# Kernel tuning notes

Hardware: AMD Instinct MI355X
Metric: run time of the kernel (lower is better)

The kernel has to match this reference:

```python
import jax, jax.numpy as jnp
import numpy as np

B, T, IN, H, NCLS = 128, 500, 306, 512, 4


def setup_inputs() -> dict:
    key = jax.random.key(0)
    ks = jax.random.split(key, 12)
    s_in = 1.0 / np.sqrt(H)  # PyTorch RNN init scale: U(-1/sqrt(H), 1/sqrt(H))
    u = lambda k, shape: jax.random.uniform(k, shape, jnp.float32, -s_in, s_in)
    return {
        "x": jax.random.normal(ks[0], (B, T, IN), jnp.float32),
        "W_ih0": u(ks[1], (H, IN)),
        "W_hh0": u(ks[2], (H, H)),
        "b_ih0": u(ks[3], (H,)),
        "b_hh0": u(ks[4], (H,)),
        "W_ih1": u(ks[5], (H, H)),
        "W_hh1": u(ks[6], (H, H)),
        "b_ih1": u(ks[7], (H,)),
        "b_hh1": u(ks[8], (H,)),
        "W_fc": u(ks[9], (NCLS, H)),
        "b_fc": u(ks[10], (NCLS,)),
    }


def _rnn_layer(inp, W_ih, W_hh, b_ih, b_hh):
    # Precompute input contribution for all timesteps: [B, T, H]
    pre = jnp.einsum('bti,hi->bth', inp, W_ih) + b_ih + b_hh
    h0 = jnp.zeros((inp.shape[0], W_hh.shape[0]), inp.dtype)

    def step(h, p_t):  # p_t: [B, H]
        h_new = jnp.tanh(p_t + h @ W_hh.T)
        return h_new, h_new

    _, hs = jax.lax.scan(step, h0, jnp.swapaxes(pre, 0, 1))  # hs: [T, B, H]
    return jnp.swapaxes(hs, 0, 1)  # [B, T, H]


def reference(x, W_ih0, W_hh0, b_ih0, b_hh0, W_ih1, W_hh1, b_ih1, b_hh1, W_fc, b_fc):
    h = _rnn_layer(x, W_ih0, W_hh0, b_ih0, b_hh0)
    h = _rnn_layer(h, W_ih1, W_hh1, b_ih1, b_hh1)
    last = h[:, -1, :]                      # [B, H]
    logits = last @ W_fc.T + b_fc           # [B, NCLS]
    return jax.nn.softmax(logits, axis=1)
```

## Files before the change

### kernel.cpp

```cpp
#include <hip/hip_runtime.h>
#include <cstdint>
#include <cstddef>

#define Bb   128
#define Tt   500
#define INn  306
#define Hh   512
#define GRID 128
#define BH32 (Bb * Hh)

typedef short bf16x8 __attribute__((ext_vector_type(8)));
typedef float f32x4  __attribute__((ext_vector_type(4)));
typedef unsigned u32x4 __attribute__((ext_vector_type(4)));
typedef unsigned short u16t;

union F8 { bf16x8 v; uint4 q; unsigned u[4]; u16t s[8]; };

__device__ __forceinline__ float bf2f(u16t h) {
  unsigned u = ((unsigned)h) << 16;
  return __builtin_bit_cast(float, u);
}
__device__ __forceinline__ u16t f2bf(float f) {
  unsigned u = __builtin_bit_cast(unsigned, f);
  unsigned r = u + 0x7fffu + ((u >> 16) & 1u);
  return (u16t)(r >> 16);
}
__device__ __forceinline__ void splitRNE(float v, u16t& hi, u16t& lo) {
  hi = f2bf(v);
  lo = f2bf(v - bf2f(hi));
}
__device__ __forceinline__ void splitTR(float v, u16t& hi, u16t& lo) {
  unsigned u = __builtin_bit_cast(unsigned, v);
  hi = (u16t)(u >> 16);
  float hf = __builtin_bit_cast(float, u & 0xFFFF0000u);
  lo = (u16t)(__builtin_bit_cast(unsigned, v - hf) >> 16);
}
__device__ __forceinline__ f32x4 MF(const F8& a, const F8& b, f32x4 c) {
  return __builtin_amdgcn_mfma_f32_16x16x32_bf16(a.v, b.v, c, 0, 0, 0);
}

__device__ __forceinline__ void stw(unsigned* p, unsigned v) {
  __hip_atomic_store(p, v, __ATOMIC_RELAXED, __HIP_MEMORY_SCOPE_AGENT);
}
__device__ __forceinline__ unsigned ldw(const unsigned* p) {
  return __hip_atomic_load(p, __ATOMIC_RELAXED, __HIP_MEMORY_SCOPE_AGENT);
}


template<bool FAST>
__device__ __forceinline__ void stf(unsigned* p, unsigned v) {
  if constexpr (FAST) *(volatile unsigned*)p = v;
  else stw(p, v);
}
template<bool FAST>
__device__ __forceinline__ void invL() {
  if constexpr (FAST) asm volatile("buffer_inv" ::: "memory");
  else asm volatile("buffer_inv sc1" ::: "memory");
}
template<bool FAST>
__device__ __forceinline__ void fpoll(const unsigned* p, unsigned v) {
  if constexpr (FAST) {
    for (;;) {
      asm volatile("buffer_inv" ::: "memory");
      if (*(const volatile unsigned*)p == v) break;
      __builtin_amdgcn_s_sleep(1);
    }
  } else {
    while (ldw(p) != v) __builtin_amdgcn_s_sleep(1);
  }
}

__device__ __forceinline__ void stage_tile(const unsigned* __restrict__ gsrc,
                                           unsigned char* smHi,
                                           unsigned char* smLo, int tid) {
  const int row = tid >> 4;
  const int c0  = tid & 15;
#pragma unroll
  for (int k = 0; k < 8; ++k) {
    const int cg = c0 + k * 16;
    const u32x4 w = *(const u32x4*)(gsrc + (size_t)row * Hh + (size_t)cg * 4);
    const unsigned hi0 = (w[1] & 0xFFFF0000u) | (w[0] >> 16);
    const unsigned hi1 = (w[3] & 0xFFFF0000u) | (w[2] >> 16);
    const unsigned lo0 = (w[1] << 16) | (w[0] & 0xFFFFu);
    const unsigned lo1 = (w[3] << 16) | (w[2] & 0xFFFFu);
    const int ch   = cg >> 1;
    const int half = cg & 1;
    const size_t boff = (size_t)row * 1024 + ((size_t)(ch ^ (row & 7)) << 4)
                      + (size_t)half * 8;
    *(uint2*)(smHi + boff) = make_uint2(hi0, hi1);
    *(uint2*)(smLo + boff) = make_uint2(lo0, lo1);
  }
}
__device__ __forceinline__ F8 fragLDS(const unsigned char* smP, int row,
                                      int kc, int quad) {
  const int c = kc * 4 + quad;
  F8 f;
  f.q = *(const uint4*)(smP + (size_t)row * 1024
                        + ((size_t)(c ^ (row & 7)) << 4));
  return f;
}

template<bool FAST>
__device__ void body(
    const float* x,
    const float* Wih0, const float* Whh0, const float* bih0, const float* bhh0,
    const float* Wih1, const float* Whh1, const float* bih1, const float* bhh1,
    const float* Wfc,  const float* bfc, float* out,
    unsigned* fl, unsigned* h0p, unsigned* h1p, unsigned char* sm,
    int sub, int tid, int Mb)
{
  const int lane = tid & 63;
  const int wave = tid >> 6;
  const int l15  = lane & 15;
  const int quad = lane >> 4;

  unsigned char* smA = sm;
  unsigned char* smB = sm + 16384;
  unsigned char* smC = sm + 32768;
  unsigned char* smD = sm + 49152;

  const bool isL0 = (sub < 8);
  const int Jb    = (isL0 ? sub : sub - 8) * 64;
  const int jn    = Jb + wave * 16 + l15;
  const int rowA  = Mb + l15;
  const int mOutB = Mb + quad * 4;

  if (isL0) {
    F8 Bxh[10], Bxl[10], Bhh[16], Bhl[16];
#pragma unroll
    for (int kc = 0; kc < 10; ++kc) {
#pragma unroll
      for (int e = 0; e < 8; ++e) {
        const int k = kc * 32 + quad * 8 + e;
        float v = (k < INn) ? Wih0[(size_t)jn * INn + k] : 0.f;
        splitRNE(v, Bxh[kc].s[e], Bxl[kc].s[e]);
      }
    }
#pragma unroll
    for (int kc = 0; kc < 16; ++kc) {
      const float* wr = Whh0 + (size_t)jn * Hh + kc * 32 + quad * 8;
#pragma unroll
      for (int e = 0; e < 8; ++e)
        splitRNE(wr[e], Bhh[kc].s[e], Bhl[kc].s[e]);
    }
    const float bv = bih0[jn] + bhh0[jn];

    for (int t = 0; t < Tt; ++t) {
      F8 xh[10], xl[10];
      {
        const float* xr = x + ((size_t)rowA * Tt + t) * INn;
#pragma unroll
        for (int kc = 0; kc < 10; ++kc) {
          const int kb = kc * 32 + quad * 8;
          float v[8];
          if (kc < 9) {
            const float2* p = (const float2*)(xr + kb);
#pragma unroll
            for (int h2 = 0; h2 < 4; ++h2) {
              float2 w = p[h2];
              v[2 * h2] = w.x; v[2 * h2 + 1] = w.y;
            }
          } else {
#pragma unroll
            for (int e = 0; e < 8; ++e)
              v[e] = (kb + e < INn) ? xr[kb + e] : 0.f;
          }
#pragma unroll
          for (int e = 0; e < 8; ++e) splitTR(v[e], xh[kc].s[e], xl[kc].s[e]);
        }
      }

      if (t >= 1) {
        asm volatile("s_waitcnt vmcnt(0)" ::: "memory");
        __syncthreads();
        if (tid == 0) stf<FAST>(fl + sub * 2 + ((t - 1) & 1), (unsigned)t);
      }
      if (t >= 1 && tid < 8)
        fpoll<FAST>(fl + tid * 2 + ((t - 1) & 1), (unsigned)t);
      if (t >= 2 && tid >= 8 && tid < 16)
        fpoll<FAST>(fl + tid * 2 + ((t - 2) & 1), (unsigned)(t - 1));
      __syncthreads();
      invL<FAST>();

      if (t >= 1) {
        stage_tile(h0p + (size_t)((t - 1) & 1) * BH32 + (size_t)Mb * Hh,
                   smA, smB, tid);
        __syncthreads();
      }
      f32x4 ac0 = {bv, bv, bv, bv};
      f32x4 ac1 = {0.f, 0.f, 0.f, 0.f};
      f32x4 ac2 = {0.f, 0.f, 0.f, 0.f};
      if (t >= 1) {
#pragma unroll
        for (int kc = 0; kc < 16; ++kc) {
          F8 ah = fragLDS(smA, l15, kc, quad);
          F8 al = fragLDS(smB, l15, kc, quad);
          ac0 = MF(ah, Bhh[kc], ac0);
          ac1 = MF(ah, Bhl[kc], ac1);
          ac2 = MF(al, Bhh[kc], ac2);
        }
      }
#pragma unroll
      for (int kc = 0; kc < 10; ++kc) {
        ac0 = MF(xh[kc], Bxh[kc], ac0);
        ac1 = MF(xh[kc], Bxl[kc], ac1);
        ac2 = MF(xl[kc], Bxh[kc], ac2);
      }

      unsigned* dst = h0p + (size_t)(t & 1) * BH32;
#pragma unroll
      for (int r = 0; r < 4; ++r) {
        const float v = tanhf(ac0[r] + ac1[r] + ac2[r]);
        u16t hb, lb; splitRNE(v, hb, lb);
        stf<FAST>(dst + (size_t)(mOutB + r) * Hh + jn,
                  ((unsigned)hb << 16) | (unsigned)lb);
      }
    }
    asm volatile("s_waitcnt vmcnt(0)" ::: "memory");
    __syncthreads();
    if (tid == 0) stf<FAST>(fl + sub * 2 + ((Tt - 1) & 1), (unsigned)Tt);
  } else {
    F8 Bih[16], Bil[16], Bh2[16], Bl2[16];
#pragma unroll
    for (int kc = 0; kc < 16; ++kc) {
      const float* w1 = Wih1 + (size_t)jn * Hh + kc * 32 + quad * 8;
      const float* w2 = Whh1 + (size_t)jn * Hh + kc * 32 + quad * 8;
#pragma unroll
      for (int e = 0; e < 8; ++e) {
        splitRNE(w1[e], Bih[kc].s[e], Bil[kc].s[e]);
        splitRNE(w2[e], Bh2[kc].s[e], Bl2[kc].s[e]);
      }
    }
    const float bv = bih1[jn] + bhh1[jn];

    for (int t = 0; t < Tt; ++t) {
      if (tid < 8)
        fpoll<FAST>(fl + tid * 2 + (t & 1), (unsigned)(t + 1));
      if (t >= 1) {
        asm volatile("s_waitcnt vmcnt(0)" ::: "memory");
        __syncthreads();
        if (tid == 0) stf<FAST>(fl + sub * 2 + ((t - 1) & 1), (unsigned)t);
        if (tid >= 8 && tid < 16)
          fpoll<FAST>(fl + tid * 2 + ((t - 1) & 1), (unsigned)t);
      }
      __syncthreads();
      invL<FAST>();

      stage_tile(h0p + (size_t)(t & 1) * BH32 + (size_t)Mb * Hh,
                 smA, smB, tid);
      if (t >= 1)
        stage_tile(h1p + (size_t)((t - 1) & 1) * BH32 + (size_t)Mb * Hh,
                   smC, smD, tid);
      __syncthreads();

      f32x4 ac0 = {bv, bv, bv, bv};
      f32x4 ac1 = {0.f, 0.f, 0.f, 0.f};
      f32x4 ac2 = {0.f, 0.f, 0.f, 0.f};
#pragma unroll
      for (int kc = 0; kc < 16; ++kc) {
        F8 ah = fragLDS(smA, l15, kc, quad);
        F8 al = fragLDS(smB, l15, kc, quad);
        ac0 = MF(ah, Bih[kc], ac0);
        ac1 = MF(ah, Bil[kc], ac1);
        ac2 = MF(al, Bih[kc], ac2);
      }
      if (t >= 1) {
#pragma unroll
        for (int kc = 0; kc < 16; ++kc) {
          F8 ah = fragLDS(smC, l15, kc, quad);
          F8 al = fragLDS(smD, l15, kc, quad);
          ac0 = MF(ah, Bh2[kc], ac0);
          ac1 = MF(ah, Bl2[kc], ac1);
          ac2 = MF(al, Bh2[kc], ac2);
        }
      }

      unsigned* dst = h1p + (size_t)(t & 1) * BH32;
#pragma unroll
      for (int r = 0; r < 4; ++r) {
        const float v = tanhf(ac0[r] + ac1[r] + ac2[r]);
        u16t hb, lb; splitRNE(v, hb, lb);
        stf<FAST>(dst + (size_t)(mOutB + r) * Hh + jn,
                  ((unsigned)hb << 16) | (unsigned)lb);
      }
    }
    asm volatile("s_waitcnt vmcnt(0)" ::: "memory");
    __syncthreads();
    if (tid == 0) stf<FAST>(fl + sub * 2 + ((Tt - 1) & 1), (unsigned)Tt);

    if (sub == 8) {
      if (tid < 8)
        fpoll<FAST>(fl + (8 + tid) * 2 + ((Tt - 1) & 1), (unsigned)Tt);
      __syncthreads();
      invL<FAST>();
      if (tid < 16) {
        const int b = Mb + tid;
        const unsigned* hp = h1p + (size_t)((Tt - 1) & 1) * BH32
                           + (size_t)b * Hh;
        float acc[4] = {bfc[0], bfc[1], bfc[2], bfc[3]};
        for (int j = 0; j < Hh; ++j) {
          const unsigned w = *(const volatile unsigned*)(hp + j);
          const float hv = bf2f((u16t)(w >> 16)) + bf2f((u16t)(w & 0xFFFFu));
#pragma unroll
          for (int cc = 0; cc < 4; ++cc) acc[cc] += hv * Wfc[cc * Hh + j];
        }
        const float mx = fmaxf(fmaxf(acc[0], acc[1]), fmaxf(acc[2], acc[3]));
        const float e0 = expf(acc[0] - mx), e1 = expf(acc[1] - mx);
        const float e2 = expf(acc[2] - mx), e3 = expf(acc[3] - mx);
        const float si = 1.f / (e0 + e1 + e2 + e3);
        out[b * 4 + 0] = e0 * si;
        out[b * 4 + 1] = e1 * si;
        out[b * 4 + 2] = e2 * si;
        out[b * 4 + 3] = e3 * si;
      }
    }
  }
}

__global__ __launch_bounds__(256, 1) void rnn_all(
    const float* x,
    const float* Wih0, const float* Whh0, const float* bih0, const float* bhh0,
    const float* Wih1, const float* Whh1, const float* bih1, const float* bhh1,
    const float* Wfc,  const float* bfc,
    float* out, unsigned char* ws)
{
  const int wg  = blockIdx.x;
  const int g   = wg & 7;
  const int sub = wg >> 3;
  const int tid = threadIdx.x;

  __shared__ __align__(16) unsigned char sm[65536];

  unsigned* fl  = (unsigned*)(ws + (size_t)g * 128);
  unsigned* h0p = (unsigned*)(ws + 1024);
  unsigned* h1p = h0p + (size_t)2 * BH32;
  const int Mb  = g * 16;

  unsigned xcc;
  asm("s_getreg_b32 %0, hwreg(HW_REG_XCC_ID)" : "=s"(xcc));
  xcc &= 7u;
  unsigned* xt = h1p + (size_t)1 * BH32 + (size_t)Mb * Hh;
  if (tid == 0) stw(xt + sub, 0xA5C30000u | xcc);
  unsigned* xsh = (unsigned*)sm;
  if (tid < 16) {
    unsigned v;
    do { v = ldw(xt + tid); } while ((v & 0xFFFFFFF8u) != 0xA5C30000u);
    xsh[tid] = v & 7u;
  }
  __syncthreads();
  bool fast = true;
  for (int i = 0; i < 16; ++i) fast = fast && (xsh[i] == xcc);
  __syncthreads();

  if (fast)
    body<true >(x, Wih0, Whh0, bih0, bhh0, Wih1, Whh1, bih1, bhh1,
                Wfc, bfc, out, fl, h0p, h1p, sm, sub, tid, Mb);
  else
    body<false>(x, Wih0, Whh0, bih0, bhh0, Wih1, Whh1, bih1, bhh1,
                Wfc, bfc, out, fl, h0p, h1p, sm, sub, tid, Mb);
}

extern "C" void kernel_launch(void* const* d_in, const int* in_sizes, int n_in,
                              void* d_out, int out_size, void* d_ws, size_t ws_size,
                              hipStream_t stream) {
  const float* x    = (const float*)d_in[0];
  const float* Wih0 = (const float*)d_in[1];
  const float* Whh0 = (const float*)d_in[2];
  const float* bih0 = (const float*)d_in[3];
  const float* bhh0 = (const float*)d_in[4];
  const float* Wih1 = (const float*)d_in[5];
  const float* Whh1 = (const float*)d_in[6];
  const float* bih1 = (const float*)d_in[7];
  const float* bhh1 = (const float*)d_in[8];
  const float* Wfc  = (const float*)d_in[9];
  const float* bfc  = (const float*)d_in[10];
  float* out = (float*)d_out;
  unsigned char* ws = (unsigned char*)d_ws;

  rnn_all<<<dim3(GRID), dim3(256), 0, stream>>>(
      x, Wih0, Whh0, bih0, bhh0, Wih1, Whh1, bih1, bhh1, Wfc, bfc, out, ws);
}
```

Before: 5.150 ms.

## Co-locate layer-0 and layer-1 waves in each workgroup with skewed wavefront schedule

Each workgroup now holds both layers: waves 0-1 compute a 32-column slice of layer 0 and waves 2-3 a 32-column slice of layer 1, with layer 1 lagging one timestep behind. All 16 workgroups in a batch group follow one uniform barrier and flag protocol over T+1 steps, and the staged h0 tile is shared by both layers through LDS. The aim is to balance work across workgroups, drop the separate two-phase polling, and reuse one staged h0 copy for both layers. In exchange each wave keeps 64 weight fragments in registers, and every workgroup now waits on all 15 peers per step.

```diff
diff --git a/kernel.cpp b/kernel.cpp
--- a/kernel.cpp
+++ b/kernel.cpp
@@ -113,27 +113,26 @@
   const int wave = tid >> 6;
   const int l15  = lane & 15;
   const int quad = lane >> 4;
+  const bool isL0 = (wave < 2);
 
   unsigned char* smA = sm;
   unsigned char* smB = sm + 16384;
   unsigned char* smC = sm + 32768;
   unsigned char* smD = sm + 49152;
 
-  const bool isL0 = (sub < 8);
-  const int Jb    = (isL0 ? sub : sub - 8) * 64;
-  const int jn    = Jb + wave * 16 + l15;
-  const int rowA  = Mb + l15;
+  const int jn    = sub * 32 + (wave & 1) * 16 + l15;
   const int mOutB = Mb + quad * 4;
 
+  F8 W[64];
+  float bv;
   if (isL0) {
-    F8 Bxh[10], Bxl[10], Bhh[16], Bhl[16];
 #pragma unroll
     for (int kc = 0; kc < 10; ++kc) {
 #pragma unroll
       for (int e = 0; e < 8; ++e) {
         const int k = kc * 32 + quad * 8 + e;
         float v = (k < INn) ? Wih0[(size_t)jn * INn + k] : 0.f;
-        splitRNE(v, Bxh[kc].s[e], Bxl[kc].s[e]);
+        splitRNE(v, W[kc].s[e], W[10 + kc].s[e]);
       }
     }
 #pragma unroll
@@ -141,178 +140,161 @@
       const float* wr = Whh0 + (size_t)jn * Hh + kc * 32 + quad * 8;
 #pragma unroll
       for (int e = 0; e < 8; ++e)
-        splitRNE(wr[e], Bhh[kc].s[e], Bhl[kc].s[e]);
-    }
-    const float bv = bih0[jn] + bhh0[jn];
-
-    for (int t = 0; t < Tt; ++t) {
-      F8 xh[10], xl[10];
-      {
-        const float* xr = x + ((size_t)rowA * Tt + t) * INn;
+        splitRNE(wr[e], W[20 + kc].s[e], W[36 + kc].s[e]);
+    }
+    bv = bih0[jn] + bhh0[jn];
+  } else {
+#pragma unroll
+    for (int kc = 0; kc < 16; ++kc) {
+      const float* w1 = Wih1 + (size_t)jn * Hh + kc * 32 + quad * 8;
+      const float* w2 = Whh1 + (size_t)jn * Hh + kc * 32 + quad * 8;
+#pragma unroll
+      for (int e = 0; e < 8; ++e) {
+        splitRNE(w1[e], W[kc].s[e], W[16 + kc].s[e]);
+        splitRNE(w2[e], W[32 + kc].s[e], W[48 + kc].s[e]);
+      }
+    }
+    bv = bih1[jn] + bhh1[jn];
+  }
+
+  const int rowA = Mb + l15;
+
+  for (int t = 0; t <= Tt; ++t) {
+    F8 xh[10], xl[10];
+    if (isL0 && t < Tt) {
+      const float* xr = x + ((size_t)rowA * Tt + t) * INn;
+#pragma unroll
+      for (int kc = 0; kc < 10; ++kc) {
+        const int kb = kc * 32 + quad * 8;
+        float v[8];
+        if (kc < 9) {
+          const float2* p = (const float2*)(xr + kb);
+#pragma unroll
+          for (int h2 = 0; h2 < 4; ++h2) {
+            float2 w = p[h2];
+            v[2 * h2] = w.x; v[2 * h2 + 1] = w.y;
+          }
+        } else {
+#pragma unroll
+          for (int e = 0; e < 8; ++e)
+            v[e] = (kb + e < INn) ? xr[kb + e] : 0.f;
+        }
+#pragma unroll
+        for (int e = 0; e < 8; ++e) splitTR(v[e], xh[kc].s[e], xl[kc].s[e]);
+      }
+    }
+
+    asm volatile("s_waitcnt vmcnt(0)" ::: "memory");
+    __syncthreads();
+    if (t >= 1 && tid == 0)
+      stf<FAST>(fl + sub * 2 + ((t - 1) & 1), (unsigned)t);
+
+    if (t >= 1 && tid < 16 && tid != sub)
+      fpoll<FAST>(fl + tid * 2 + ((t - 1) & 1), (unsigned)t);
+    __syncthreads();
+    invL<FAST>();
+
+    if (t >= 1)
+      stage_tile(h0p + (size_t)((t - 1) & 1) * BH32 + (size_t)Mb * Hh,
+                 smA, smB, tid);
+    if (t >= 2)
+      stage_tile(h1p + (size_t)((t - 2) & 1) * BH32 + (size_t)Mb * Hh,
+                 smC, smD, tid);
+    __syncthreads();
+
+    if (isL0) {
+      if (t < Tt) {
+        f32x4 ac0 = {bv, bv, bv, bv};
+        f32x4 ac1 = {0.f, 0.f, 0.f, 0.f};
+        f32x4 ac2 = {0.f, 0.f, 0.f, 0.f};
+        if (t >= 1) {
+#pragma unroll
+          for (int kc = 0; kc < 16; ++kc) {
+            F8 ah = fragLDS(smA, l15, kc, quad);
+            F8 al = fragLDS(smB, l15, kc, quad);
+            ac0 = MF(ah, W[20 + kc], ac0);
+            ac1 = MF(ah, W[36 + kc], ac1);
+            ac2 = MF(al, W[20 + kc], ac2);
+          }
+        }
 #pragma unroll
         for (int kc = 0; kc < 10; ++kc) {
-          const int kb = kc * 32 + quad * 8;
-          float v[8];
-          if (kc < 9) {
-            const float2* p = (const float2*)(xr + kb);
-#pragma unroll
-            for (int h2 = 0; h2 < 4; ++h2) {
-              float2 w = p[h2];
-              v[2 * h2] = w.x; v[2 * h2 + 1] = w.y;
-            }
-          } else {
-#pragma unroll
-            for (int e = 0; e < 8; ++e)
-              v[e] = (kb + e < INn) ? xr[kb + e] : 0.f;
-          }
-#pragma unroll
-          for (int e = 0; e < 8; ++e) splitTR(v[e], xh[kc].s[e], xl[kc].s[e]);
-        }
-      }
-
+          ac0 = MF(xh[kc], W[kc], ac0);
+          ac1 = MF(xh[kc], W[10 + kc], ac1);
+          ac2 = MF(xl[kc], W[kc], ac2);
+        }
+        unsigned* dst = h0p + (size_t)(t & 1) * BH32;
+#pragma unroll
+        for (int r = 0; r < 4; ++r) {
+          const float v = tanhf(ac0[r] + ac1[r] + ac2[r]);
+          u16t hb, lb; splitRNE(v, hb, lb);
+          stf<FAST>(dst + (size_t)(mOutB + r) * Hh + jn,
+                    ((unsigned)hb << 16) | (unsigned)lb);
+        }
+      }
+    } else {
       if (t >= 1) {
-        asm volatile("s_waitcnt vmcnt(0)" ::: "memory");
-        __syncthreads();
-        if (tid == 0) stf<FAST>(fl + sub * 2 + ((t - 1) & 1), (unsigned)t);
-      }
-      if (t >= 1 && tid < 8)
-        fpoll<FAST>(fl + tid * 2 + ((t - 1) & 1), (unsigned)t);
-      if (t >= 2 && tid >= 8 && tid < 16)
-        fpoll<FAST>(fl + tid * 2 + ((t - 2) & 1), (unsigned)(t - 1));
-      __syncthreads();
-      invL<FAST>();
-
-      if (t >= 1) {
-        stage_tile(h0p + (size_t)((t - 1) & 1) * BH32 + (size_t)Mb * Hh,
-                   smA, smB, tid);
-        __syncthreads();
-      }
-      f32x4 ac0 = {bv, bv, bv, bv};
-      f32x4 ac1 = {0.f, 0.f, 0.f, 0.f};
-      f32x4 ac2 = {0.f, 0.f, 0.f, 0.f};
-      if (t >= 1) {
+        f32x4 ac0 = {bv, bv, bv, bv};
+        f32x4 ac1 = {0.f, 0.f, 0.f, 0.f};
+        f32x4 ac2 = {0.f, 0.f, 0.f, 0.f};
 #pragma unroll
         for (int kc = 0; kc < 16; ++kc) {
           F8 ah = fragLDS(smA, l15, kc, quad);
           F8 al = fragLDS(smB, l15, kc, quad);
-          ac0 = MF(ah, Bhh[kc], ac0);
-          ac1 = MF(ah, Bhl[kc], ac1);
-          ac2 = MF(al, Bhh[kc], ac2);
-        }
-      }
-#pragma unroll
-      for (int kc = 0; kc < 10; ++kc) {
-        ac0 = MF(xh[kc], Bxh[kc], ac0);
-        ac1 = MF(xh[kc], Bxl[kc], ac1);
-        ac2 = MF(xl[kc], Bxh[kc], ac2);
-      }
-
-      unsigned* dst = h0p + (size_t)(t & 1) * BH32;
-#pragma unroll
-      for (int r = 0; r < 4; ++r) {
-        const float v = tanhf(ac0[r] + ac1[r] + ac2[r]);
-        u16t hb, lb; splitRNE(v, hb, lb);
-        stf<FAST>(dst + (size_t)(mOutB + r) * Hh + jn,
-                  ((unsigned)hb << 16) | (unsigned)lb);
-      }
-    }
-    asm volatile("s_waitcnt vmcnt(0)" ::: "memory");
+          ac0 = MF(ah, W[kc], ac0);
+          ac1 = MF(ah, W[16 + kc], ac1);
+          ac2 = MF(al, W[kc], ac2);
+        }
+        if (t >= 2) {
+#pragma unroll
+          for (int kc = 0; kc < 16; ++kc) {
+            F8 ah = fragLDS(smC, l15, kc, quad);
+            F8 al = fragLDS(smD, l15, kc, quad);
+            ac0 = MF(ah, W[32 + kc], ac0);
+            ac1 = MF(ah, W[48 + kc], ac1);
+            ac2 = MF(al, W[32 + kc], ac2);
+          }
+        }
+        unsigned* dst = h1p + (size_t)((t - 1) & 1) * BH32;
+#pragma unroll
+        for (int r = 0; r < 4; ++r) {
+          const float v = tanhf(ac0[r] + ac1[r] + ac2[r]);
+          u16t hb, lb; splitRNE(v, hb, lb);
+          stf<FAST>(dst + (size_t)(mOutB + r) * Hh + jn,
+                    ((unsigned)hb << 16) | (unsigned)lb);
+        }
+      }
+    }
+  }
+
+  asm volatile("s_waitcnt vmcnt(0)" ::: "memory");
+  __syncthreads();
+  if (tid == 0) stf<FAST>(fl + sub * 2 + (Tt & 1), (unsigned)(Tt + 1));
+
+  if (sub == 0) {
+    if (tid < 16 && tid != 0)
+      fpoll<FAST>(fl + tid * 2 + (Tt & 1), (unsigned)(Tt + 1));
     __syncthreads();
-    if (tid == 0) stf<FAST>(fl + sub * 2 + ((Tt - 1) & 1), (unsigned)Tt);
-  } else {
-    F8 Bih[16], Bil[16], Bh2[16], Bl2[16];
-#pragma unroll
-    for (int kc = 0; kc < 16; ++kc) {
-      const float* w1 = Wih1 + (size_t)jn * Hh + kc * 32 + quad * 8;
-      const float* w2 = Whh1 + (size_t)jn * Hh + kc * 32 + quad * 8;
-#pragma unroll
-      for (int e = 0; e < 8; ++e) {
-        splitRNE(w1[e], Bih[kc].s[e], Bil[kc].s[e]);
-        splitRNE(w2[e], Bh2[kc].s[e], Bl2[kc].s[e]);
-      }
-    }
-    const float bv = bih1[jn] + bhh1[jn];
-
-    for (int t = 0; t < Tt; ++t) {
-      if (tid < 8)
-        fpoll<FAST>(fl + tid * 2 + (t & 1), (unsigned)(t + 1));
-      if (t >= 1) {
-        asm volatile("s_waitcnt vmcnt(0)" ::: "memory");
-        __syncthreads();
-        if (tid == 0) stf<FAST>(fl + sub * 2 + ((t - 1) & 1), (unsigned)t);
-        if (tid >= 8 && tid < 16)
-          fpoll<FAST>(fl + tid * 2 + ((t - 1) & 1), (unsigned)t);
-      }
-      __syncthreads();
-      invL<FAST>();
-
-      stage_tile(h0p + (size_t)(t & 1) * BH32 + (size_t)Mb * Hh,
-                 smA, smB, tid);
-      if (t >= 1)
-        stage_tile(h1p + (size_t)((t - 1) & 1) * BH32 + (size_t)Mb * Hh,
-                   smC, smD, tid);
-      __syncthreads();
-
-      f32x4 ac0 = {bv, bv, bv, bv};
-      f32x4 ac1 = {0.f, 0.f, 0.f, 0.f};
-      f32x4 ac2 = {0.f, 0.f, 0.f, 0.f};
-#pragma unroll
-      for (int kc = 0; kc < 16; ++kc) {
-        F8 ah = fragLDS(smA, l15, kc, quad);
-        F8 al = fragLDS(smB, l15, kc, quad);
-        ac0 = MF(ah, Bih[kc], ac0);
-        ac1 = MF(ah, Bil[kc], ac1);
-        ac2 = MF(al, Bih[kc], ac2);
-      }
-      if (t >= 1) {
-#pragma unroll
-        for (int kc = 0; kc < 16; ++kc) {
-          F8 ah = fragLDS(smC, l15, kc, quad);
-          F8 al = fragLDS(smD, l15, kc, quad);
-          ac0 = MF(ah, Bh2[kc], ac0);
-          ac1 = MF(ah, Bl2[kc], ac1);
-          ac2 = MF(al, Bh2[kc], ac2);
-        }
-      }
-
-      unsigned* dst = h1p + (size_t)(t & 1) * BH32;
-#pragma unroll
-      for (int r = 0; r < 4; ++r) {
-        const float v = tanhf(ac0[r] + ac1[r] + ac2[r]);
-        u16t hb, lb; splitRNE(v, hb, lb);
-        stf<FAST>(dst + (size_t)(mOutB + r) * Hh + jn,
-                  ((unsigned)hb << 16) | (unsigned)lb);
-      }
-    }
-    asm volatile("s_waitcnt vmcnt(0)" ::: "memory");
-    __syncthreads();
-    if (tid == 0) stf<FAST>(fl + sub * 2 + ((Tt - 1) & 1), (unsigned)Tt);
-
-    if (sub == 8) {
-      if (tid < 8)
-        fpoll<FAST>(fl + (8 + tid) * 2 + ((Tt - 1) & 1), (unsigned)Tt);
-      __syncthreads();
-      invL<FAST>();
-      if (tid < 16) {
-        const int b = Mb + tid;
-        const unsigned* hp = h1p + (size_t)((Tt - 1) & 1) * BH32
-                           + (size_t)b * Hh;
-        float acc[4] = {bfc[0], bfc[1], bfc[2], bfc[3]};
-        for (int j = 0; j < Hh; ++j) {
-          const unsigned w = *(const volatile unsigned*)(hp + j);
-          const float hv = bf2f((u16t)(w >> 16)) + bf2f((u16t)(w & 0xFFFFu));
-#pragma unroll
-          for (int cc = 0; cc < 4; ++cc) acc[cc] += hv * Wfc[cc * Hh + j];
-        }
-        const float mx = fmaxf(fmaxf(acc[0], acc[1]), fmaxf(acc[2], acc[3]));
-        const float e0 = expf(acc[0] - mx), e1 = expf(acc[1] - mx);
-        const float e2 = expf(acc[2] - mx), e3 = expf(acc[3] - mx);
-        const float si = 1.f / (e0 + e1 + e2 + e3);
-        out[b * 4 + 0] = e0 * si;
-        out[b * 4 + 1] = e1 * si;
-        out[b * 4 + 2] = e2 * si;
-        out[b * 4 + 3] = e3 * si;
-      }
+    invL<FAST>();
+    if (tid < 16) {
+      const int b = Mb + tid;
+      const unsigned* hp = h1p + (size_t)((Tt - 1) & 1) * BH32
+                         + (size_t)b * Hh;
+      float acc[4] = {bfc[0], bfc[1], bfc[2], bfc[3]};
+      for (int j = 0; j < Hh; ++j) {
+        const unsigned w = *(const volatile unsigned*)(hp + j);
+        const float hv = bf2f((u16t)(w >> 16)) + bf2f((u16t)(w & 0xFFFFu));
+#pragma unroll
+        for (int cc = 0; cc < 4; ++cc) acc[cc] += hv * Wfc[cc * Hh + j];
+      }
+      const float mx = fmaxf(fmaxf(acc[0], acc[1]), fmaxf(acc[2], acc[3]));
+      const float e0 = expf(acc[0] - mx), e1 = expf(acc[1] - mx);
+      const float e2 = expf(acc[2] - mx), e3 = expf(acc[3] - mx);
+      const float si = 1.f / (e0 + e1 + e2 + e3);
+      out[b * 4 + 0] = e0 * si;
+      out[b * 4 + 1] = e1 * si;
+      out[b * 4 + 2] = e2 * si;
+      out[b * 4 + 3] = e3 * si;
     }
   }
 }
```

Measured after the change: 5.507 ms. 6.9% more time.
